# Kernel tuning notes

Hardware: AMD Instinct MI355X
Metric: run time of the kernel (lower is better)

The kernel has to match this reference:

```python
import jax, jax.numpy as jnp
import numpy as np

V, C, T, H, L, B = 32000, 1024, 1024, 16, 4, 4
HD = C // H
FF = 4 * C
LN_EPS = 1e-5


def _sinusoidal(block_size, n_embd):
    pos = np.arange(block_size, dtype=np.float32)[:, None]
    div = np.exp(np.arange(0, n_embd, 2, dtype=np.float32) * (-np.log(10000.0) / n_embd))
    enc = np.zeros((block_size, n_embd), dtype=np.float32)
    enc[:, 0::2] = np.sin(pos * div)
    enc[:, 1::2] = np.cos(pos * div)
    return jnp.asarray(enc)


def setup_inputs() -> dict:
    key = jax.random.key(0)
    ks = jax.random.split(key, 12)
    std = 0.02
    n = lambda k, s: jax.random.normal(k, s, jnp.float32) * std
    return {
        'idx': jax.random.randint(ks[0], (B, T), 0, V),
        'emb': n(ks[1], (V, C)),
        'pos_enc': _sinusoidal(T, C),
        'Wq': n(ks[2], (L, C, C)),
        'Wk': n(ks[3], (L, C, C)),
        'Wv': n(ks[4], (L, C, C)),
        'Wo': n(ks[5], (L, C, C)),
        'bo': jnp.zeros((L, C), jnp.float32),
        'W1': n(ks[6], (L, C, FF)),
        'b1': jnp.zeros((L, FF), jnp.float32),
        'W2': n(ks[7], (L, FF, C)),
        'b2': jnp.zeros((L, C), jnp.float32),
        'ln1_g': jnp.ones((L, C), jnp.float32),
        'ln1_b': jnp.zeros((L, C), jnp.float32),
        'ln2_g': jnp.ones((L, C), jnp.float32),
        'ln2_b': jnp.zeros((L, C), jnp.float32),
        'lnf_g': jnp.ones((C,), jnp.float32),
        'lnf_b': jnp.zeros((C,), jnp.float32),
        'Wlm': n(ks[8], (C, V)),
        'blm': jnp.zeros((V,), jnp.float32),
    }


def _layer_norm(x, g, b):
    m = jnp.mean(x, -1, keepdims=True)
    v = jnp.var(x, -1, keepdims=True)
    return (x - m) * jax.lax.rsqrt(v + LN_EPS) * g + b


def _forward(idx, emb, pos_enc, Wq, Wk, Wv, Wo, bo, W1, b1, W2, b2,
             ln1_g, ln1_b, ln2_g, ln2_b, lnf_g, lnf_b, Wlm, blm):
    Bv, Tv = idx.shape
    x = emb[idx] + pos_enc[None, :Tv, :]  # [B,T,C]
    mask = jnp.tril(jnp.ones((Tv, Tv), dtype=bool))
    scale = HD ** -0.5

    def block(x, p):
        wq, wk, wv, wo, bov, w1, b1v, w2, b2v, g1, bn1, g2, bn2 = p
        h = _layer_norm(x, g1, bn1)
        q = jnp.einsum('btc,chd->bhtd', h, wq.reshape(C, H, HD))
        k = jnp.einsum('btc,chd->bhtd', h, wk.reshape(C, H, HD))
        v = jnp.einsum('btc,chd->bhtd', h, wv.reshape(C, H, HD))
        wei = jnp.einsum('bhqd,bhkd->bhqk', q, k) * scale
        wei = jnp.where(mask, wei, -jnp.inf)
        wei = jax.nn.softmax(wei, axis=-1)
        o = jnp.einsum('bhqk,bhkd->bhqd', wei, v)
        o = o.transpose(0, 2, 1, 3).reshape(Bv, Tv, C)
        x = x + o @ wo + bov
        h2 = _layer_norm(x, g2, bn2)
        x = x + jax.nn.gelu(h2 @ w1 + b1v, approximate=False) @ w2 + b2v
        return x, None

    x, _ = jax.lax.scan(block, x, (Wq, Wk, Wv, Wo, bo, W1, b1, W2, b2,
                                   ln1_g, ln1_b, ln2_g, ln2_b))
    x = _layer_norm(x, lnf_g, lnf_b)
    return x @ Wlm + blm  # [B,T,V]


def reference(idx, emb, pos_enc, Wq, Wk, Wv, Wo, bo, W1, b1, W2, b2,
              ln1_g, ln1_b, ln2_g, ln2_b, lnf_g, lnf_b, Wlm, blm):
    return _forward(idx, emb, pos_enc, Wq, Wk, Wv, Wo, bo, W1, b1, W2, b2,
                    ln1_g, ln1_b, ln2_g, ln2_b, lnf_g, lnf_b, Wlm, blm)
```

## Files before the change

### kernel.cpp

```cpp
#include <hip/hip_runtime.h>

#define V_  32000
#define C_  1024
#define T_  1024
#define H_  16
#define L_  4
#define B_  4
#define HD_ 64
#define FF_ 4096
#define M_  (B_ * T_)

typedef __attribute__((ext_vector_type(8))) short bf16x8;
typedef __attribute__((ext_vector_type(4))) float f32x4;
typedef unsigned short u16;

#define FENCE() asm volatile("" ::: "memory")
#define BAR()  do { FENCE(); __builtin_amdgcn_s_barrier(); FENCE(); } while (0)
#define VMW(n) asm volatile("s_waitcnt vmcnt(" #n ")" ::: "memory")

__device__ __forceinline__ u16 f2bf(float f) {
  unsigned u = __builtin_bit_cast(unsigned, f);
  u += 0x7fffu + ((u >> 16) & 1u);
  return (u16)(u >> 16);
}

__device__ __forceinline__ float gelu_f(float v) {
  return 0.5f * v * (1.0f + erff(v * 0.70710678118654752f));
}

__device__ __forceinline__ void gload16(const u16* g, u16* l) {
  __builtin_amdgcn_global_load_lds(
      (const __attribute__((address_space(1))) void*)g,
      (__attribute__((address_space(3))) void*)l, 16, 0, 0);
}

template <int FUSE_LN>
__global__ __launch_bounds__(256)
void embed_kernel(const int* __restrict__ idx, const float* __restrict__ emb,
                  const float* __restrict__ pos, float* __restrict__ x,
                  const float* __restrict__ g, const float* __restrict__ bta,
                  u16* __restrict__ hout) {
  int row = blockIdx.x;
  int t = row & (T_ - 1);
  int tok = idx[row];
  float4 e = reinterpret_cast<const float4*>(emb + (size_t)tok * C_)[threadIdx.x];
  float4 p = reinterpret_cast<const float4*>(pos + (size_t)t * C_)[threadIdx.x];
  float4 r;
  r.x = e.x + p.x; r.y = e.y + p.y; r.z = e.z + p.z; r.w = e.w + p.w;
  reinterpret_cast<float4*>(x + (size_t)row * C_)[threadIdx.x] = r;
  if constexpr (FUSE_LN) {
    int tid = threadIdx.x;
    float s  = r.x + r.y + r.z + r.w;
    float ss = r.x * r.x + r.y * r.y + r.z * r.z + r.w * r.w;
    #pragma unroll
    for (int d = 1; d < 64; d <<= 1) {
      s  += __shfl_xor(s, d, 64);
      ss += __shfl_xor(ss, d, 64);
    }
    __shared__ float rs[4], rss[4];
    int w = tid >> 6, lane = tid & 63;
    if (lane == 0) { rs[w] = s; rss[w] = ss; }
    __syncthreads();
    s  = rs[0] + rs[1] + rs[2] + rs[3];
    ss = rss[0] + rss[1] + rss[2] + rss[3];
    float mean = s * (1.0f / C_);
    float var  = ss * (1.0f / C_) - mean * mean;
    float rstd = rsqrtf(var + 1e-5f);
    float4 gv = reinterpret_cast<const float4*>(g)[tid];
    float4 bv = reinterpret_cast<const float4*>(bta)[tid];
    union { u16 u[4]; uint2 v; } pk;
    pk.u[0] = f2bf((r.x - mean) * rstd * gv.x + bv.x);
    pk.u[1] = f2bf((r.y - mean) * rstd * gv.y + bv.y);
    pk.u[2] = f2bf((r.z - mean) * rstd * gv.z + bv.z);
    pk.u[3] = f2bf((r.w - mean) * rstd * gv.w + bv.w);
    *reinterpret_cast<uint2*>(&hout[(size_t)row * C_ + tid * 4]) = pk.v;
  }
}

__global__ __launch_bounds__(256)
void ln_kernel(const float* __restrict__ xin, const float* __restrict__ g,
               const float* __restrict__ bta, u16* __restrict__ out) {
  const int w = threadIdx.x >> 6, lane = threadIdx.x & 63;
  const int row = blockIdx.x * 4 + w;
  const float4* xr = reinterpret_cast<const float4*>(xin + (size_t)row * C_);
  float4 xv[4];
  float s = 0.f, ss = 0.f;
  #pragma unroll
  for (int j = 0; j < 4; ++j) {
    xv[j] = xr[lane + 64 * j];
    s  += xv[j].x + xv[j].y + xv[j].z + xv[j].w;
    ss += xv[j].x * xv[j].x + xv[j].y * xv[j].y + xv[j].z * xv[j].z + xv[j].w * xv[j].w;
  }
  #pragma unroll
  for (int d = 1; d < 64; d <<= 1) {
    s  += __shfl_xor(s, d, 64);
    ss += __shfl_xor(ss, d, 64);
  }
  float mean = s * (1.0f / C_);
  float var  = ss * (1.0f / C_) - mean * mean;
  float rstd = rsqrtf(var + 1e-5f);
  #pragma unroll
  for (int j = 0; j < 4; ++j) {
    float4 gv = reinterpret_cast<const float4*>(g)[lane + 64 * j];
    float4 bv = reinterpret_cast<const float4*>(bta)[lane + 64 * j];
    union { u16 u[4]; uint2 v; } pk;
    pk.u[0] = f2bf((xv[j].x - mean) * rstd * gv.x + bv.x);
    pk.u[1] = f2bf((xv[j].y - mean) * rstd * gv.y + bv.y);
    pk.u[2] = f2bf((xv[j].z - mean) * rstd * gv.z + bv.z);
    pk.u[3] = f2bf((xv[j].w - mean) * rstd * gv.w + bv.w);
    *reinterpret_cast<uint2*>(&out[(size_t)row * C_ + (lane + 64 * j) * 4]) = pk.v;
  }
}

__global__ __launch_bounds__(256)
void wtrans_kernel(const float* __restrict__ W, u16* __restrict__ Wt, int K, int N,
                   size_t dstBS) {
  const float* src = W + (size_t)blockIdx.z * K * N;
  u16* dst = Wt + (size_t)blockIdx.z * dstBS;
  __shared__ float tile[32][33];
  int k0 = blockIdx.y * 32, n0 = blockIdx.x * 32;
  int tx = threadIdx.x & 31, ty = threadIdx.x >> 5;
  #pragma unroll
  for (int i = 0; i < 4; ++i)
    tile[ty * 4 + i][tx] = src[(size_t)(k0 + ty * 4 + i) * N + n0 + tx];
  __syncthreads();
  int n = threadIdx.x >> 3, q = threadIdx.x & 7;
  union { u16 u[4]; uint2 v; } pk;
  #pragma unroll
  for (int j = 0; j < 4; ++j) pk.u[j] = f2bf(tile[4 * q + j][n]);
  *reinterpret_cast<uint2*>(&dst[(size_t)(n0 + n) * K + k0 + 4 * q]) = pk.v;
}

__global__ __launch_bounds__(256)
void wtrans4_kernel(const float* __restrict__ Wq, const float* __restrict__ Wk,
                    const float* __restrict__ Wv, const float* __restrict__ Wo,
                    u16* __restrict__ WqkvT, u16* __restrict__ WoT) {
  int zz = blockIdx.z;
  int l = zz & 3, which = zz >> 2;
  const float* src = (which == 0 ? Wq : which == 1 ? Wk : which == 2 ? Wv : Wo)
                     + (size_t)l * C_ * C_;
  u16* dst = (which == 3)
      ? WoT + (size_t)l * C_ * C_
      : WqkvT + (size_t)l * 3 * C_ * C_ + (size_t)which * C_ * C_;
  __shared__ float tile[32][33];
  int k0 = blockIdx.y * 32, n0 = blockIdx.x * 32;
  int tx = threadIdx.x & 31, ty = threadIdx.x >> 5;
  #pragma unroll
  for (int i = 0; i < 4; ++i)
    tile[ty * 4 + i][tx] = src[(size_t)(k0 + ty * 4 + i) * C_ + n0 + tx];
  __syncthreads();
  int n = threadIdx.x >> 3, q = threadIdx.x & 7;
  union { u16 u[4]; uint2 v; } pk;
  #pragma unroll
  for (int j = 0; j < 4; ++j) pk.u[j] = f2bf(tile[4 * q + j][n]);
  *reinterpret_cast<uint2*>(&dst[(size_t)(n0 + n) * C_ + k0 + 4 * q]) = pk.v;
}

template <int MODE, int GROUP_M>
__global__ __launch_bounds__(256)
void gemm_bt(const u16* __restrict__ A, const u16* __restrict__ Bt,
             const float* __restrict__ bias, const float* __restrict__ resid,
             void* __restrict__ Cout, u16* __restrict__ vtb,
             int M, int N, int K) {
  __shared__ u16 smem[4][4096];
  const int nbm = M >> 7, nbn = N >> 7;
  const int nwg = nbm * nbn;
  const int bid = blockIdx.x;
  const int chunk = nwg >> 3;
  const int swz = (bid & 7) * chunk + (bid >> 3);
  const int gsz = GROUP_M * nbn;
  const int grp = swz / gsz, rem = swz % gsz;
  const int by = grp * GROUP_M + (rem % GROUP_M);
  const int bx = rem / GROUP_M;
  const int m0 = by * 128, n0 = bx * 128;

  const int tid = threadIdx.x, lane = tid & 63, w = tid >> 6;
  const int wr = w >> 1, wc = w & 1;
  const int frow = lane & 15, fk = (lane >> 4) * 8;
  const int srow = lane >> 2, scol = (lane & 3) * 8;

  f32x4 acc[4][4];
  #pragma unroll
  for (int i = 0; i < 4; ++i)
    #pragma unroll
    for (int j = 0; j < 4; ++j) acc[i][j] = (f32x4)0.0f;

  auto stage = [&](int d, int k0) {
    gload16(&A [(size_t)(m0 + w * 32 +      srow) * K + k0 + scol], smem[d] + w * 1024);
    gload16(&A [(size_t)(m0 + w * 32 + 16 + srow) * K + k0 + scol], smem[d] + w * 1024 + 512);
    gload16(&Bt[(size_t)(n0 + w * 32 +      srow) * K + k0 + scol], smem[2 + d] + w * 1024);
    gload16(&Bt[(size_t)(n0 + w * 32 + 16 + srow) * K + k0 + scol], smem[2 + d] + w * 1024 + 512);
  };

  const int NT = K >> 5;
  stage(0, 0);
  VMW(0); BAR();

  for (int kt = 0; kt < NT; ++kt) {
    const int cur = kt & 1;
    if (kt + 1 < NT) stage(cur ^ 1, (kt + 1) << 5);

    bf16x8 af[4], bfr[4];
    #pragma unroll
    for (int mi = 0; mi < 4; ++mi)
      af[mi] = *reinterpret_cast<const bf16x8*>(&smem[cur][(wr * 64 + mi * 16 + frow) * 32 + fk]);
    #pragma unroll
    for (int ni = 0; ni < 4; ++ni)
      bfr[ni] = *reinterpret_cast<const bf16x8*>(&smem[2 + cur][(wc * 64 + ni * 16 + frow) * 32 + fk]);
    #pragma unroll
    for (int mi = 0; mi < 4; ++mi)
      #pragma unroll
      for (int ni = 0; ni < 4; ++ni)
        acc[mi][ni] = __builtin_amdgcn_mfma_f32_16x16x32_bf16(af[mi], bfr[ni], acc[mi][ni], 0, 0, 0);

    VMW(0); BAR();
  }

  u16* outb = (u16*)Cout;
  float* outf = (float*)Cout;

  if constexpr (MODE == 1) {
    char* ef = (char*)smem;
    #pragma unroll
    for (int h = 0; h < 2; ++h) {
      if (wr == h) {
        #pragma unroll
        for (int mi = 0; mi < 4; ++mi)
          #pragma unroll
          for (int ni = 0; ni < 4; ++ni) {
            int rl0 = mi * 16 + ((lane >> 4) << 2);
            int cl = wc * 64 + ni * 16 + (lane & 15);
            #pragma unroll
            for (int r = 0; r < 4; ++r) {
              int rl = rl0 + r;
              *(float*)(ef + rl * 512 + ((cl * 4) ^ ((rl & 7) << 4))) = acc[mi][ni][r];
            }
          }
      }
      BAR();
      {
        int row = tid >> 2;
        int s = (row & 7) << 4;
        #pragma unroll
        for (int j = 0; j < 8; ++j) {
          int g = (tid & 3) + 4 * j;
          float4 v = *reinterpret_cast<float4*>(ef + row * 512 + ((g * 16) ^ s));
          int ocol = n0 + g * 4;
          float4 bv4 = *reinterpret_cast<const float4*>(&bias[ocol]);
          size_t off = (size_t)(m0 + h * 64 + row) * N + ocol;
          float4 rv = *reinterpret_cast<const float4*>(&resid[off]);
          float4 o;
          o.x = v.x + bv4.x + rv.x; o.y = v.y + bv4.y + rv.y;
          o.z = v.z + bv4.z + rv.z; o.w = v.w + bv4.w + rv.w;
          *reinterpret_cast<float4*>(&outf[off]) = o;
        }
      }
      BAR();
    }
    return;
  }

  const bool vblk = (MODE == 4) && (n0 >= 2 * C_);
  #pragma unroll
  for (int mi = 0; mi < 4; ++mi) {
    #pragma unroll
    for (int ni = 0; ni < 4; ++ni) {
      int orow = m0 + wr * 64 + mi * 16 + ((lane >> 4) << 2);
      int ocol = n0 + wc * 64 + ni * 16 + (lane & 15);
      float bv = 0.0f;
      if constexpr (MODE == 2 || MODE == 3) bv = bias[ocol];
      if constexpr (MODE == 4) {
        if (vblk) {
          int vcol = ocol - 2 * C_;
          int hh = vcol >> 6, d = vcol & 63;
          int bb = orow >> 10, t0 = orow & (T_ - 1);
          union { u16 u[4]; uint2 v2; } pk;
          #pragma unroll
          for (int r = 0; r < 4; ++r) pk.u[r] = f2bf(acc[mi][ni][r]);
          *reinterpret_cast<uint2*>(
              &vtb[(((size_t)bb * H_ + hh) * HD_ + d) * T_ + t0]) = pk.v2;
        } else {
          #pragma unroll
          for (int r = 0; r < 4; ++r)
            outb[(size_t)(orow + r) * (2 * C_) + ocol] = f2bf(acc[mi][ni][r]);
        }
      } else {
        #pragma unroll
        for (int r = 0; r < 4; ++r) {
          size_t off = (size_t)(orow + r) * N + ocol;
          float val = acc[mi][ni][r] + bv;
          if constexpr (MODE == 0) {
            outb[off] = f2bf(val);
          } else if constexpr (MODE == 2) {
            outb[off] = f2bf(gelu_f(val));
          } else if constexpr (MODE == 3) {
            outf[off] = val;
          }
        }
      }
    }
  }
}

template <int MODE>
__global__ __launch_bounds__(512, 2)
void gemm8(const u16* __restrict__ A, const u16* __restrict__ Bt,
           const float* __restrict__ bias, const float* __restrict__ resid,
           void* __restrict__ Cout, int M, int N, int K) {
  __shared__ u16 lds8[65536];
  const int nbm = M >> 8, nbn = N >> 8;
  const int nwg = nbm * nbn;
  const int chunk = nwg >> 3;
  const int bid = blockIdx.x;
  const int swz = (bid & 7) * chunk + (bid >> 3);
  const int gsz = 4 * nbn;
  const int grp = swz / gsz, rem = swz % gsz;
  const int by = grp * 4 + (rem & 3);
  const int bx = rem >> 2;
  const int m0 = by << 8, n0 = bx << 8;

  const int tid = threadIdx.x, lane = tid & 63, w = tid >> 6;
  const int wm = w >> 2, wn = w & 3;
  const int fr = lane & 15, kgb = (lane >> 4) * 16;
  const int scolz = 8 * ((lane & 7) ^ (lane >> 3));
  const int NT = K >> 6;
  const int NI = NT >> 1;

  f32x4 acc[8][4];
  #pragma unroll
  for (int i = 0; i < 8; ++i)
    #pragma unroll
    for (int j = 0; j < 4; ++j) acc[i][j] = (f32x4)0.0f;

  auto ldr = [&](int d, int isB, int row, int cb) -> bf16x8 {
    int bo = row * 128 + (cb ^ ((row & 7) << 4));
    const char* base = (const char*)lds8 + d * 65536 + isB * 32768 +
                       (isB ? (wn >> 1) : wm) * 16384;
    return *reinterpret_cast<const bf16x8*>(base + bo);
  };
  auto stage_half = [&](const u16* grow0, u16* ldst) {
    #pragma unroll
    for (int p = 0; p < 2; ++p) {
      int r = (p * 8 + w) * 8 + (lane >> 3);
      gload16(grow0 + (size_t)r * K + scolz, ldst + (p * 8 + w) * 512);
    }
  };
  auto stageA = [&](int d, int h, int t) {
    stage_half(&A[(size_t)(m0 + h * 128) * K + t * 64],
               lds8 + d * 32768 + h * 8192);
  };
  auto stageB = [&](int d, int h, int t) {
    stage_half(&Bt[(size_t)(n0 + h * 128) * K + t * 64],
               lds8 + d * 32768 + 16384 + h * 8192);
  };

  bf16x8 af[2][2], bfr[4][2];

#define LDA_Q(d, q) do {                                   \
    af[0][0] = ldr(d, 0, (q) * 32 + fr,      kgb);         \
    af[0][1] = ldr(d, 0, (q) * 32 + fr,      64 + kgb);    \
    af[1][0] = ldr(d, 0, (q) * 32 + 16 + fr, kgb);         \
    af[1][1] = ldr(d, 0, (q) * 32 + 16 + fr, 64 + kgb);    \
  } while (0)
#define LDB_ALL(d) do {                                    \
    _Pragma("unroll")                                      \
    for (int nj = 0; nj < 4; ++nj) {                       \
      bfr[nj][0] = ldr(d, 1, (wn & 1) * 64 + nj * 16 + fr, kgb);      \
      bfr[nj][1] = ldr(d, 1, (wn & 1) * 64 + nj * 16 + fr, 64 + kgb); \
    }                                                      \
  } while (0)
#define MFMA_Q(q) do {                                     \
    __builtin_amdgcn_s_setprio(1);                         \
    _Pragma("unroll")                                      \
    for (int lmi = 0; lmi < 2; ++lmi)                      \
      _Pragma("unroll")                                    \
      for (int nj = 0; nj < 4; ++nj)                       \
        _Pragma("unroll")                                  \
        for (int ks = 0; ks < 2; ++ks)                     \
          acc[2 * (q) + lmi][nj] = __builtin_amdgcn_mfma_f32_16x16x32_bf16( \
              af[lmi][ks], bfr[nj][ks], acc[2 * (q) + lmi][nj], 0, 0, 0);   \
    __builtin_amdgcn_s_setprio(0);                         \
  } while (0)

  stageB(0, 0, 0); stageB(0, 1, 0);
  stageA(0, 0, 0); stageA(0, 1, 0);
  stageB(1, 0, 1); stageB(1, 1, 1);
  VMW(4);
  BAR();

  for (int i = 0; i < NI; ++i) {
    const int a = 2 * i, b = 2 * i + 1;
    const bool pa = (a + 2 < NT), pb = (b + 2 < NT);
    LDB_ALL(0); LDA_Q(0, 0);
    stageA(1, 0, b);
    BAR(); MFMA_Q(0); BAR();
    LDA_Q(0, 1);
    stageA(1, 1, b);
    if (pa) stageB(0, 0, a + 2);
    BAR(); MFMA_Q(1); BAR();
    LDA_Q(0, 2);
    if (pa) stageB(0, 1, a + 2);
    BAR(); MFMA_Q(2); BAR();
    LDA_Q(0, 3);
    BAR(); MFMA_Q(3);
    if (pa) { VMW(4); } else { VMW(0); }
    BAR();
    LDB_ALL(1); LDA_Q(1, 0);
    if (pa) stageA(0, 0, a + 2);
    BAR(); MFMA_Q(0); BAR();
    LDA_Q(1, 1);
    if (pa) stageA(0, 1, a + 2);
    BAR(); MFMA_Q(1); BAR();
    LDA_Q(1, 2);
    if (pb) stageB(1, 0, b + 2);
    BAR(); MFMA_Q(2); BAR();
    LDA_Q(1, 3);
    if (pb) stageB(1, 1, b + 2);
    BAR(); MFMA_Q(3);
    if (pb) { VMW(4); } else { VMW(0); }
    BAR();
  }
#undef LDA_Q
#undef LDB_ALL
#undef MFMA_Q

  u16* outb = (u16*)Cout;
  float* outf = (float*)Cout;
  char* ef = (char*)lds8;
  #pragma unroll
  for (int h = 0; h < 2; ++h) {
    if (wm == h) {
      #pragma unroll
      for (int mi = 0; mi < 8; ++mi)
        #pragma unroll
        for (int nj = 0; nj < 4; ++nj) {
          int rl0 = mi * 16 + ((lane >> 4) << 2);
          int cl = wn * 64 + nj * 16 + (lane & 15);
          #pragma unroll
          for (int r = 0; r < 4; ++r) {
            int rl = rl0 + r;
            *(float*)(ef + rl * 1024 + ((cl * 4) ^ ((rl & 7) << 4))) = acc[mi][nj][r];
          }
        }
    }
    BAR();
    {
      int row = tid >> 2;
      int s = (row & 7) << 4;
      #pragma unroll
      for (int j = 0; j < 8; ++j) {
        int g = (tid & 3) + 4 * j;
        float4 v0 = *reinterpret_cast<float4*>(ef + row * 1024 + ((g * 32) ^ s));
        float4 v1 = *reinterpret_cast<float4*>(ef + row * 1024 + ((g * 32 + 16) ^ s));
        int ocol = n0 + g * 8;
        float4 b0 = *reinterpret_cast<const float4*>(&bias[ocol]);
        float4 b1 = *reinterpret_cast<const float4*>(&bias[ocol + 4]);
        size_t off = (size_t)(m0 + h * 128 + row) * N + ocol;
        if constexpr (MODE == 3) {
          float4 o0, o1;
          o0.x = v0.x + b0.x; o0.y = v0.y + b0.y; o0.z = v0.z + b0.z; o0.w = v0.w + b0.w;
          o1.x = v1.x + b1.x; o1.y = v1.y + b1.y; o1.z = v1.z + b1.z; o1.w = v1.w + b1.w;
          *reinterpret_cast<float4*>(&outf[off]) = o0;
          *reinterpret_cast<float4*>(&outf[off + 4]) = o1;
        } else {
          union { u16 u[8]; uint4 q; } pk;
          pk.u[0] = f2bf(gelu_f(v0.x + b0.x));
          pk.u[1] = f2bf(gelu_f(v0.y + b0.y));
          pk.u[2] = f2bf(gelu_f(v0.z + b0.z));
          pk.u[3] = f2bf(gelu_f(v0.w + b0.w));
          pk.u[4] = f2bf(gelu_f(v1.x + b1.x));
          pk.u[5] = f2bf(gelu_f(v1.y + b1.y));
          pk.u[6] = f2bf(gelu_f(v1.z + b1.z));
          pk.u[7] = f2bf(gelu_f(v1.w + b1.w));
          *reinterpret_cast<uint4*>(&outb[off]) = pk.q;
        }
      }
    }
    BAR();
  }
}

template <int MODE>
__global__ __launch_bounds__(256)
void gemm_legacy(const u16* __restrict__ A, const float* __restrict__ Bw,
                 const float* __restrict__ bias, const float* __restrict__ resid,
                 void* __restrict__ Cout, int M, int N, int K) {
  __shared__ u16 As[128][40];
  __shared__ u16 Bs[128][40];
  const int m0 = blockIdx.y * 128, n0 = blockIdx.x * 128;
  const int tid = threadIdx.x, lane = tid & 63, w = tid >> 6;
  const int wr = w >> 1, wc = w & 1;
  const int row = lane & 15, kk8 = (lane >> 4) * 8;
  f32x4 acc[4][4];
  #pragma unroll
  for (int i = 0; i < 4; ++i)
    #pragma unroll
    for (int j = 0; j < 4; ++j) acc[i][j] = (f32x4)0.0f;
  for (int k0 = 0; k0 < K; k0 += 32) {
    #pragma unroll
    for (int i = 0; i < 2; ++i) {
      int e = (tid + i * 256) * 8;
      int r = e >> 5, c = e & 31;
      *reinterpret_cast<uint4*>(&As[r][c]) =
        *reinterpret_cast<const uint4*>(&A[(size_t)(m0 + r) * K + k0 + c]);
    }
    #pragma unroll
    for (int i = 0; i < 4; ++i) {
      int e = (tid + i * 256) * 4;
      int kr = e >> 7, c = e & 127;
      float4 bv = *reinterpret_cast<const float4*>(&Bw[(size_t)(k0 + kr) * N + n0 + c]);
      Bs[c + 0][kr] = f2bf(bv.x);
      Bs[c + 1][kr] = f2bf(bv.y);
      Bs[c + 2][kr] = f2bf(bv.z);
      Bs[c + 3][kr] = f2bf(bv.w);
    }
    __syncthreads();
    bf16x8 af[4], bfr[4];
    #pragma unroll
    for (int mi = 0; mi < 4; ++mi)
      af[mi] = *reinterpret_cast<const bf16x8*>(&As[wr * 64 + mi * 16 + row][kk8]);
    #pragma unroll
    for (int ni = 0; ni < 4; ++ni)
      bfr[ni] = *reinterpret_cast<const bf16x8*>(&Bs[wc * 64 + ni * 16 + row][kk8]);
    #pragma unroll
    for (int mi = 0; mi < 4; ++mi)
      #pragma unroll
      for (int ni = 0; ni < 4; ++ni)
        acc[mi][ni] = __builtin_amdgcn_mfma_f32_16x16x32_bf16(af[mi], bfr[ni], acc[mi][ni], 0, 0, 0);
    __syncthreads();
  }
  u16* outb = (u16*)Cout;
  float* outf = (float*)Cout;
  #pragma unroll
  for (int mi = 0; mi < 4; ++mi) {
    #pragma unroll
    for (int ni = 0; ni < 4; ++ni) {
      int orow = m0 + wr * 64 + mi * 16 + ((lane >> 4) << 2);
      int ocol = n0 + wc * 64 + ni * 16 + (lane & 15);
      float bv = 0.0f;
      if constexpr (MODE != 0) bv = bias[ocol];
      #pragma unroll
      for (int r = 0; r < 4; ++r) {
        size_t off = (size_t)(orow + r) * N + ocol;
        float val = acc[mi][ni][r] + bv;
        if constexpr (MODE == 0) outb[off] = f2bf(val);
        else if constexpr (MODE == 1) outf[off] = val + resid[off];
        else if constexpr (MODE == 2) {
          outb[off] = f2bf(gelu_f(val));
        } else outf[off] = val;
      }
    }
  }
}

__global__ __launch_bounds__(512)
void attn_kernel(const u16* __restrict__ qg, const u16* __restrict__ kg,
                 const u16* __restrict__ vt, u16* __restrict__ og) {
  const int bh = blockIdx.y;
  const int q0 = blockIdx.x * 128;
  const int b = bh >> 4;
  const int tid = threadIdx.x, lane = tid & 63, w = tid >> 6;
  const int fr = lane & 15, kk8 = (lane >> 4) * 8;
  __shared__ u16 KS[2][4096];
  __shared__ u16 VS[2][4096];
  __shared__ u16 Ps[8][16][72];

  const int ldq = 2 * C_;
  const size_t baseq = ((size_t)b * T_) * ldq + (bh & 15) * HD_;
  const u16* qbase = qg + baseq;
  const u16* kbase = kg + baseq;
  const u16* vbase = vt + ((size_t)bh * HD_) * T_;
  const size_t baseo = ((size_t)b * T_) * C_ + (bh & 15) * HD_;
  const int qw = q0 + w * 16;

  bf16x8 qf[2];
  #pragma unroll
  for (int s = 0; s < 2; ++s)
    qf[s] = *reinterpret_cast<const bf16x8*>(&qbase[(size_t)(qw + fr) * ldq + s * 32 + kk8]);

  const int srow8 = lane >> 3;
  const int scol = 8 * ((lane & 7) ^ srow8);
  auto stageKV = [&](int d, int kv0) {
    int rr = w * 8 + srow8;
    gload16(kbase + (size_t)(kv0 + rr) * ldq + scol, &KS[d][w * 512]);
    gload16(vbase + (size_t)rr * T_ + kv0 + scol,    &VS[d][w * 512]);
  };
  auto ldS = [&](const u16* base, int row, int cu) -> bf16x8 {
    return *reinterpret_cast<const bf16x8*>(&base[row * 64 + (cu ^ ((row & 7) << 3))]);
  };

  f32x4 acc_o[4];
  #pragma unroll
  for (int dt = 0; dt < 4; ++dt) acc_o[dt] = (f32x4)0.0f;
  float m_run[4] = {-1e30f, -1e30f, -1e30f, -1e30f};
  float l_run[4] = {0.f, 0.f, 0.f, 0.f};
  const float scale = 0.125f;

  const int kv_end = q0 + 128;
  stageKV(0, 0);
  VMW(0); BAR();

  int cur = 0;
  for (int kv0 = 0; kv0 < kv_end; kv0 += 64, cur ^= 1) {
    if (kv0 + 64 < kv_end) stageKV(cur ^ 1, kv0 + 64);

    f32x4 sacc[4];
    #pragma unroll
    for (int nt = 0; nt < 4; ++nt) sacc[nt] = (f32x4)0.0f;
    #pragma unroll
    for (int nt = 0; nt < 4; ++nt)
      #pragma unroll
      for (int s = 0; s < 2; ++s) {
        bf16x8 kf = ldS(KS[cur], nt * 16 + fr, s * 32 + kk8);
        sacc[nt] = __builtin_amdgcn_mfma_f32_16x16x32_bf16(qf[s], kf, sacc[nt], 0, 0, 0);
      }

    #pragma unroll
    for (int i = 0; i < 4; ++i) {
      int qrow = qw + ((lane >> 4) << 2) + i;
      float sv[4], pv[4];
      #pragma unroll
      for (int nt = 0; nt < 4; ++nt) {
        sv[nt] = sacc[nt][i] * scale;
        if (kv0 + nt * 16 + (lane & 15) > qrow) sv[nt] = -1e30f;
      }
      float mx = fmaxf(fmaxf(sv[0], sv[1]), fmaxf(sv[2], sv[3]));
      #pragma unroll
      for (int d = 1; d < 16; d <<= 1) mx = fmaxf(mx, __shfl_xor(mx, d, 64));
      float mnew = fmaxf(m_run[i], mx);
      float rsum = 0.0f;
      #pragma unroll
      for (int nt = 0; nt < 4; ++nt) { pv[nt] = __expf(sv[nt] - mnew); rsum += pv[nt]; }
      float alpha = __expf(m_run[i] - mnew);
      #pragma unroll
      for (int d = 1; d < 16; d <<= 1) rsum += __shfl_xor(rsum, d, 64);
      l_run[i] = l_run[i] * alpha + rsum;
      m_run[i] = mnew;
      #pragma unroll
      for (int dt = 0; dt < 4; ++dt) acc_o[dt][i] *= alpha;
      #pragma unroll
      for (int nt = 0; nt < 4; ++nt)
        Ps[w][((lane >> 4) << 2) + i][(lane & 15) + nt * 16] = f2bf(pv[nt]);
    }

    #pragma unroll
    for (int dt = 0; dt < 4; ++dt)
      #pragma unroll
      for (int s = 0; s < 2; ++s) {
        bf16x8 pf = *reinterpret_cast<const bf16x8*>(&Ps[w][fr][s * 32 + kk8]);
        bf16x8 vf = ldS(VS[cur], dt * 16 + fr, s * 32 + kk8);
        acc_o[dt] = __builtin_amdgcn_mfma_f32_16x16x32_bf16(pf, vf, acc_o[dt], 0, 0, 0);
      }
    VMW(0); BAR();
  }

  #pragma unroll
  for (int dt = 0; dt < 4; ++dt)
    #pragma unroll
    for (int i = 0; i < 4; ++i) {
      int r = qw + ((lane >> 4) << 2) + i;
      float val = acc_o[dt][i] / l_run[i];
      og[baseo + (size_t)r * C_ + dt * 16 + (lane & 15)] = f2bf(val);
    }
}

__global__ __launch_bounds__(256)
void attn_legacy(const u16* __restrict__ qg, const u16* __restrict__ kg,
                 const u16* __restrict__ vg, u16* __restrict__ og, int ldq) {
  const int bh = blockIdx.y;
  const int b = bh >> 4, hh = bh & 15;
  const int q0 = blockIdx.x * 64;
  const int tid = threadIdx.x, lane = tid & 63, w = tid >> 6;
  const int row = lane & 15, kk8 = (lane >> 4) * 8;
  __shared__ u16 Ks[64][72];
  __shared__ u16 Vt[64][72];
  __shared__ u16 Ps[4][16][72];

  const size_t basei = ((size_t)b * T_) * ldq + hh * HD_;
  const size_t baseo = ((size_t)b * T_) * C_ + hh * HD_;
  const int qw = q0 + w * 16;

  bf16x8 qf[2];
  #pragma unroll
  for (int s = 0; s < 2; ++s)
    qf[s] = *reinterpret_cast<const bf16x8*>(&qg[basei + (size_t)(qw + row) * ldq + s * 32 + kk8]);

  f32x4 acc_o[4];
  #pragma unroll
  for (int dt = 0; dt < 4; ++dt) acc_o[dt] = (f32x4)0.0f;
  float m_run[4] = {-1e30f, -1e30f, -1e30f, -1e30f};
  float l_run[4] = {0.f, 0.f, 0.f, 0.f};
  const float scale = 0.125f;

  const int sc = (tid & 7) * 8;
  const int kv_end = q0 + 64;
  for (int kv0 = 0; kv0 < kv_end; kv0 += 64) {
    #pragma unroll
    for (int p = 0; p < 2; ++p) {
      int sr = p * 32 + (tid >> 3);
      *reinterpret_cast<uint4*>(&Ks[sr][sc]) =
        *reinterpret_cast<const uint4*>(&kg[basei + (size_t)(kv0 + sr) * ldq + sc]);
      union { uint4 u4; u16 us[8]; } vv;
      vv.u4 = *reinterpret_cast<const uint4*>(&vg[basei + (size_t)(kv0 + sr) * ldq + sc]);
      #pragma unroll
      for (int j = 0; j < 8; ++j) Vt[sc + j][sr] = vv.us[j];
    }
    __syncthreads();

    f32x4 sacc[4];
    #pragma unroll
    for (int nt = 0; nt < 4; ++nt) sacc[nt] = (f32x4)0.0f;
    #pragma unroll
    for (int nt = 0; nt < 4; ++nt)
      #pragma unroll
      for (int s = 0; s < 2; ++s) {
        bf16x8 kf = *reinterpret_cast<const bf16x8*>(&Ks[nt * 16 + row][s * 32 + kk8]);
        sacc[nt] = __builtin_amdgcn_mfma_f32_16x16x32_bf16(qf[s], kf, sacc[nt], 0, 0, 0);
      }

    #pragma unroll
    for (int i = 0; i < 4; ++i) {
      int qrow = qw + ((lane >> 4) << 2) + i;
      float sv[4], pv[4];
      #pragma unroll
      for (int nt = 0; nt < 4; ++nt) {
        sv[nt] = sacc[nt][i] * scale;
        if (kv0 + nt * 16 + (lane & 15) > qrow) sv[nt] = -1e30f;
      }
      float mx = fmaxf(fmaxf(sv[0], sv[1]), fmaxf(sv[2], sv[3]));
      #pragma unroll
      for (int d = 1; d < 16; d <<= 1) mx = fmaxf(mx, __shfl_xor(mx, d, 64));
      float mnew = fmaxf(m_run[i], mx);
      float rsum = 0.0f;
      #pragma unroll
      for (int nt = 0; nt < 4; ++nt) { pv[nt] = __expf(sv[nt] - mnew); rsum += pv[nt]; }
      float alpha = __expf(m_run[i] - mnew);
      #pragma unroll
      for (int d = 1; d < 16; d <<= 1) rsum += __shfl_xor(rsum, d, 64);
      l_run[i] = l_run[i] * alpha + rsum;
      m_run[i] = mnew;
      #pragma unroll
      for (int dt = 0; dt < 4; ++dt) acc_o[dt][i] *= alpha;
      #pragma unroll
      for (int nt = 0; nt < 4; ++nt)
        Ps[w][((lane >> 4) << 2) + i][(lane & 15) + nt * 16] = f2bf(pv[nt]);
    }

    #pragma unroll
    for (int dt = 0; dt < 4; ++dt)
      #pragma unroll
      for (int s = 0; s < 2; ++s) {
        bf16x8 pf = *reinterpret_cast<const bf16x8*>(&Ps[w][row][s * 32 + kk8]);
        bf16x8 vf = *reinterpret_cast<const bf16x8*>(&Vt[dt * 16 + row][s * 32 + kk8]);
        acc_o[dt] = __builtin_amdgcn_mfma_f32_16x16x32_bf16(pf, vf, acc_o[dt], 0, 0, 0);
      }
    __syncthreads();
  }

  #pragma unroll
  for (int dt = 0; dt < 4; ++dt)
    #pragma unroll
    for (int i = 0; i < 4; ++i) {
      int r = qw + ((lane >> 4) << 2) + i;
      float val = acc_o[dt][i] / l_run[i];
      og[baseo + (size_t)r * C_ + dt * 16 + (lane & 15)] = f2bf(val);
    }
}

extern "C" void kernel_launch(void* const* d_in, const int* in_sizes, int n_in,
                              void* d_out, int out_size, void* d_ws, size_t ws_size,
                              hipStream_t stream) {
  const int*   idx  = (const int*)d_in[0];
  const float* emb  = (const float*)d_in[1];
  const float* pos  = (const float*)d_in[2];
  const float* Wq   = (const float*)d_in[3];
  const float* Wk   = (const float*)d_in[4];
  const float* Wv   = (const float*)d_in[5];
  const float* Wo   = (const float*)d_in[6];
  const float* bo   = (const float*)d_in[7];
  const float* W1   = (const float*)d_in[8];
  const float* b1   = (const float*)d_in[9];
  const float* W2   = (const float*)d_in[10];
  const float* b2   = (const float*)d_in[11];
  const float* ln1g = (const float*)d_in[12];
  const float* ln1b = (const float*)d_in[13];
  const float* ln2g = (const float*)d_in[14];
  const float* ln2b = (const float*)d_in[15];
  const float* lnfg = (const float*)d_in[16];
  const float* lnfb = (const float*)d_in[17];
  const float* Wlm  = (const float*)d_in[18];
  const float* blm  = (const float*)d_in[19];

  char* ws = (char*)d_ws;
  float* x    = (float*)ws;
  u16*   h    = (u16*)(ws + (16u << 20));
  u16*   qkv  = (u16*)(ws + (24u << 20));
  u16*   vtb  = (u16*)(ws + (40u << 20));
  u16*   ob   = (u16*)(ws + (48u << 20));
  u16*   ffb  = (u16*)(ws + (24u << 20));

  u16* WqkvT = (u16*)(ws + (56u  << 20));
  u16* WoT   = (u16*)(ws + (80u  << 20));
  u16* W1T   = (u16*)(ws + (88u  << 20));
  u16* W2T   = (u16*)(ws + (120u << 20));
  u16* WlmT  = (u16*)(ws + (152u << 20));
  const size_t WS_NEED = (152ull << 20) + 2ull * C_ * V_;

  dim3 blk(256), blk8(512), blkA(512);
  const int nQKV = (M_ / 128) * (3 * C_ / 128);
  const int nCC  = (M_ / 128) * (C_ / 128);
  const int nF1_8 = (M_ / 256) * (FF_ / 256);
  const int nLM_8 = (M_ / 256) * (V_ / 256);
  dim3 gA(T_ / 128, B_ * H_);

  if (ws_size >= WS_NEED) {
    const size_t s3 = (size_t)3 * C_ * C_;
    embed_kernel<1><<<M_, blk, 0, stream>>>(idx, emb, pos, x, ln1g, ln1b, h);
    wtrans4_kernel<<<dim3(C_ / 32, C_ / 32, 16), blk, 0, stream>>>(Wq, Wk, Wv, Wo, WqkvT, WoT);
    wtrans_kernel<<<dim3(FF_ / 32, C_ / 32, L_), blk, 0, stream>>>(W1, W1T, C_, FF_, (size_t)C_ * FF_);
    wtrans_kernel<<<dim3(C_ / 32, FF_ / 32, L_), blk, 0, stream>>>(W2, W2T, FF_, C_, (size_t)C_ * FF_);
    wtrans_kernel<<<dim3(V_ / 32,  C_ / 32, 1),  blk, 0, stream>>>(Wlm, WlmT, C_, V_, (size_t)C_ * V_);

    for (int l = 0; l < L_; ++l) {
      if (l > 0)
        ln_kernel<<<M_ / 4, blk, 0, stream>>>(x, ln1g + l * C_, ln1b + l * C_, h);
      gemm_bt<4, 8><<<nQKV, blk, 0, stream>>>(h, WqkvT + (size_t)l * s3, nullptr, nullptr, qkv, vtb, M_, 3 * C_, C_);
      attn_kernel<<<gA, blkA, 0, stream>>>(qkv, qkv + C_, vtb, ob);
      gemm_bt<1, 8><<<nCC, blk, 0, stream>>>(ob, WoT + (size_t)l * C_ * C_, bo + l * C_, x, x, nullptr, M_, C_, C_);
      ln_kernel<<<M_ / 4, blk, 0, stream>>>(x, ln2g + l * C_, ln2b + l * C_, h);
      gemm8<2><<<nF1_8, blk8, 0, stream>>>(h, W1T + (size_t)l * C_ * FF_, b1 + l * FF_, nullptr, ffb, M_, FF_, C_);
      gemm_bt<1, 8><<<nCC, blk, 0, stream>>>(ffb, W2T + (size_t)l * C_ * FF_, b2 + l * C_, x, x, nullptr, M_, C_, FF_);
    }
    ln_kernel<<<M_ / 4, blk, 0, stream>>>(x, lnfg, lnfb, h);
    gemm8<3><<<nLM_8, blk8, 0, stream>>>(h, WlmT, blm, nullptr, (float*)d_out, M_, V_, C_);
  } else {
    embed_kernel<0><<<M_, blk, 0, stream>>>(idx, emb, pos, x, nullptr, nullptr, nullptr);
    float* xr = x;
    u16* qb = qkv;
    u16* kb = qkv + (size_t)M_ * C_;
    u16* vb = (u16*)(ws + (40u << 20));
    dim3 gC(C_ / 128, M_ / 128);
    dim3 gF(FF_ / 128, M_ / 128);
    dim3 gV(V_ / 128, M_ / 128);
    dim3 gAl(T_ / 64, B_ * H_);
    for (int l = 0; l < L_; ++l) {
      ln_kernel<<<M_ / 4, blk, 0, stream>>>(xr, ln1g + l * C_, ln1b + l * C_, h);
      gemm_legacy<0><<<gC, blk, 0, stream>>>(h, Wq + (size_t)l * C_ * C_, nullptr, nullptr, qb, M_, C_, C_);
      gemm_legacy<0><<<gC, blk, 0, stream>>>(h, Wk + (size_t)l * C_ * C_, nullptr, nullptr, kb, M_, C_, C_);
      gemm_legacy<0><<<gC, blk, 0, stream>>>(h, Wv + (size_t)l * C_ * C_, nullptr, nullptr, vb, M_, C_, C_);
      attn_legacy<<<gAl, blk, 0, stream>>>(qb, kb, vb, ob, C_);
      gemm_legacy<1><<<gC, blk, 0, stream>>>(ob, Wo + (size_t)l * C_ * C_, bo + l * C_, xr, xr, M_, C_, C_);
      ln_kernel<<<M_ / 4, blk, 0, stream>>>(xr, ln2g + l * C_, ln2b + l * C_, h);
      gemm_legacy<2><<<gF, blk, 0, stream>>>(h, W1 + (size_t)l * C_ * FF_, b1 + l * FF_, nullptr, ffb, M_, FF_, C_);
      gemm_legacy<1><<<gC, blk, 0, stream>>>(ffb, W2 + (size_t)l * FF_ * C_, b2 + l * C_, xr, xr, M_, C_, FF_);
    }
    ln_kernel<<<M_ / 4, blk, 0, stream>>>(xr, lnfg, lnfb, h);
    gemm_legacy<3><<<gV, blk, 0, stream>>>(h, Wlm, blm, nullptr, (float*)d_out, M_, V_, C_);
  }
}
```

Before: 1.516 ms.

## Stage QK epilogue through LDS, revert gemm8 epilogue to direct stores

The MODE 4 (QKV) GEMM epilogue for Q/K columns now converts to bf16, stages the tile through swizzled LDS and writes 16-byte coalesced rows instead of scattered 2-byte stores. The 256x256 gemm8 kernel drops its LDS-staged, vectorised epilogue in favour of direct per-element global stores, adding a MODE 1 residual path. In attention, the alpha rescale of the output accumulator is moved after the P stores to LDS. The changes pull in opposite directions: the QKV store gets more coalesced, while gemm8 stores become scattered scalar writes.

```diff
diff --git a/kernel.cpp b/kernel.cpp
--- a/kernel.cpp
+++ b/kernel.cpp
@@ -260,17 +260,37 @@
     return;
   }
 
-  const bool vblk = (MODE == 4) && (n0 >= 2 * C_);
-  #pragma unroll
-  for (int mi = 0; mi < 4; ++mi) {
-    #pragma unroll
-    for (int ni = 0; ni < 4; ++ni) {
-      int orow = m0 + wr * 64 + mi * 16 + ((lane >> 4) << 2);
-      int ocol = n0 + wc * 64 + ni * 16 + (lane & 15);
-      float bv = 0.0f;
-      if constexpr (MODE == 2 || MODE == 3) bv = bias[ocol];
-      if constexpr (MODE == 4) {
-        if (vblk) {
+  if constexpr (MODE == 4) {
+    const bool vblk = (n0 >= 2 * C_);
+    if (!vblk) {
+      char* ef = (char*)smem;
+      #pragma unroll
+      for (int mi = 0; mi < 4; ++mi)
+        #pragma unroll
+        for (int ni = 0; ni < 4; ++ni) {
+          int rl0 = wr * 64 + mi * 16 + ((lane >> 4) << 2);
+          int cl = wc * 64 + ni * 16 + (lane & 15);
+          #pragma unroll
+          for (int r = 0; r < 4; ++r) {
+            int rl = rl0 + r;
+            *(u16*)(ef + rl * 256 + ((cl * 2) ^ ((rl & 7) << 4))) = f2bf(acc[mi][ni][r]);
+          }
+        }
+      BAR();
+      int cc = tid & 15;
+      #pragma unroll
+      for (int j = 0; j < 8; ++j) {
+        int rr = (tid >> 4) + 16 * j;
+        uint4 v = *reinterpret_cast<uint4*>(ef + rr * 256 + ((cc * 16) ^ ((rr & 7) << 4)));
+        *reinterpret_cast<uint4*>(&outb[(size_t)(m0 + rr) * (2 * C_) + n0 + cc * 8]) = v;
+      }
+    } else {
+      #pragma unroll
+      for (int mi = 0; mi < 4; ++mi)
+        #pragma unroll
+        for (int ni = 0; ni < 4; ++ni) {
+          int orow = m0 + wr * 64 + mi * 16 + ((lane >> 4) << 2);
+          int ocol = n0 + wc * 64 + ni * 16 + (lane & 15);
           int vcol = ocol - 2 * C_;
           int hh = vcol >> 6, d = vcol & 63;
           int bb = orow >> 10, t0 = orow & (T_ - 1);
@@ -279,23 +299,29 @@
           for (int r = 0; r < 4; ++r) pk.u[r] = f2bf(acc[mi][ni][r]);
           *reinterpret_cast<uint2*>(
               &vtb[(((size_t)bb * H_ + hh) * HD_ + d) * T_ + t0]) = pk.v2;
-        } else {
-          #pragma unroll
-          for (int r = 0; r < 4; ++r)
-            outb[(size_t)(orow + r) * (2 * C_) + ocol] = f2bf(acc[mi][ni][r]);
         }
-      } else {
-        #pragma unroll
-        for (int r = 0; r < 4; ++r) {
-          size_t off = (size_t)(orow + r) * N + ocol;
-          float val = acc[mi][ni][r] + bv;
-          if constexpr (MODE == 0) {
-            outb[off] = f2bf(val);
-          } else if constexpr (MODE == 2) {
-            outb[off] = f2bf(gelu_f(val));
-          } else if constexpr (MODE == 3) {
-            outf[off] = val;
-          }
+    }
+    return;
+  }
+
+  #pragma unroll
+  for (int mi = 0; mi < 4; ++mi) {
+    #pragma unroll
+    for (int ni = 0; ni < 4; ++ni) {
+      int orow = m0 + wr * 64 + mi * 16 + ((lane >> 4) << 2);
+      int ocol = n0 + wc * 64 + ni * 16 + (lane & 15);
+      float bv = 0.0f;
+      if constexpr (MODE == 2 || MODE == 3) bv = bias[ocol];
+      #pragma unroll
+      for (int r = 0; r < 4; ++r) {
+        size_t off = (size_t)(orow + r) * N + ocol;
+        float val = acc[mi][ni][r] + bv;
+        if constexpr (MODE == 0) {
+          outb[off] = f2bf(val);
+        } else if constexpr (MODE == 2) {
+          outb[off] = f2bf(gelu_f(val));
+        } else if constexpr (MODE == 3) {
+          outf[off] = val;
         }
       }
     }
@@ -426,57 +452,29 @@
 
   u16* outb = (u16*)Cout;
   float* outf = (float*)Cout;
-  char* ef = (char*)lds8;
-  #pragma unroll
-  for (int h = 0; h < 2; ++h) {
-    if (wm == h) {
-      #pragma unroll
-      for (int mi = 0; mi < 8; ++mi)
-        #pragma unroll
-        for (int nj = 0; nj < 4; ++nj) {
-          int rl0 = mi * 16 + ((lane >> 4) << 2);
-          int cl = wn * 64 + nj * 16 + (lane & 15);
-          #pragma unroll
-          for (int r = 0; r < 4; ++r) {
-            int rl = rl0 + r;
-            *(float*)(ef + rl * 1024 + ((cl * 4) ^ ((rl & 7) << 4))) = acc[mi][nj][r];
-          }
+  #pragma unroll
+  for (int mi = 0; mi < 8; ++mi) {
+    #pragma unroll
+    for (int nj = 0; nj < 4; ++nj) {
+      int orow = m0 + wm * 128 + mi * 16 + ((lane >> 4) << 2);
+      int ocol = n0 + wn * 64 + nj * 16 + (lane & 15);
+      float bv = 0.0f;
+      if constexpr (MODE != 0) bv = bias[ocol];
+      #pragma unroll
+      for (int r = 0; r < 4; ++r) {
+        size_t off = (size_t)(orow + r) * N + ocol;
+        float val = acc[mi][nj][r] + bv;
+        if constexpr (MODE == 0) {
+          outb[off] = f2bf(val);
+        } else if constexpr (MODE == 1) {
+          outf[off] = val + resid[off];
+        } else if constexpr (MODE == 2) {
+          outb[off] = f2bf(gelu_f(val));
+        } else {
+          outf[off] = val;
         }
-    }
-    BAR();
-    {
-      int row = tid >> 2;
-      int s = (row & 7) << 4;
-      #pragma unroll
-      for (int j = 0; j < 8; ++j) {
-        int g = (tid & 3) + 4 * j;
-        float4 v0 = *reinterpret_cast<float4*>(ef + row * 1024 + ((g * 32) ^ s));
-        float4 v1 = *reinterpret_cast<float4*>(ef + row * 1024 + ((g * 32 + 16) ^ s));
-        int ocol = n0 + g * 8;
-        float4 b0 = *reinterpret_cast<const float4*>(&bias[ocol]);
-        float4 b1 = *reinterpret_cast<const float4*>(&bias[ocol + 4]);
-        size_t off = (size_t)(m0 + h * 128 + row) * N + ocol;
-        if constexpr (MODE == 3) {
-          float4 o0, o1;
-          o0.x = v0.x + b0.x; o0.y = v0.y + b0.y; o0.z = v0.z + b0.z; o0.w = v0.w + b0.w;
-          o1.x = v1.x + b1.x; o1.y = v1.y + b1.y; o1.z = v1.z + b1.z; o1.w = v1.w + b1.w;
-          *reinterpret_cast<float4*>(&outf[off]) = o0;
-          *reinterpret_cast<float4*>(&outf[off + 4]) = o1;
-        } else {
-          union { u16 u[8]; uint4 q; } pk;
-          pk.u[0] = f2bf(gelu_f(v0.x + b0.x));
-          pk.u[1] = f2bf(gelu_f(v0.y + b0.y));
-          pk.u[2] = f2bf(gelu_f(v0.z + b0.z));
-          pk.u[3] = f2bf(gelu_f(v0.w + b0.w));
-          pk.u[4] = f2bf(gelu_f(v1.x + b1.x));
-          pk.u[5] = f2bf(gelu_f(v1.y + b1.y));
-          pk.u[6] = f2bf(gelu_f(v1.z + b1.z));
-          pk.u[7] = f2bf(gelu_f(v1.w + b1.w));
-          *reinterpret_cast<uint4*>(&outb[off]) = pk.q;
-        }
-      }
-    }
-    BAR();
+      }
+    }
   }
 }
 
@@ -740,10 +738,10 @@
       l_run[i] = l_run[i] * alpha + rsum;
       m_run[i] = mnew;
       #pragma unroll
-      for (int dt = 0; dt < 4; ++dt) acc_o[dt][i] *= alpha;
-      #pragma unroll
       for (int nt = 0; nt < 4; ++nt)
         Ps[w][((lane >> 4) << 2) + i][(lane & 15) + nt * 16] = f2bf(pv[nt]);
+      #pragma unroll
+      for (int dt = 0; dt < 4; ++dt) acc_o[dt][i] *= alpha;
     }
 
     #pragma unroll
```

Result: faster. 1.483 ms (-2.2%).
